# Kernel tuning notes

Hardware: AMD Instinct MI355X
Metric: run time of the kernel (lower is better)

## Reference

```python
import jax, jax.numpy as jnp
import numpy as np

B, L, D, H = 2, 4096, 768, 12
Dh = D // H


def setup_inputs() -> dict:
    key = jax.random.key(0)
    k1, k2, k3 = jax.random.split(key, 3)
    x = jax.random.normal(k1, (B, L, D), dtype=jnp.float32)
    Wqkv = jax.random.normal(k2, (D, 3 * D), dtype=jnp.float32) * 0.02
    bqkv = jnp.zeros((3 * D,), dtype=jnp.float32)
    Wo = jax.random.normal(k3, (D, D), dtype=jnp.float32) * 0.02
    bo = jnp.zeros((D,), dtype=jnp.float32)
    return {"x": x, "Wqkv": Wqkv, "bqkv": bqkv, "Wo": Wo, "bo": bo}


def reference(x, Wqkv, bqkv, Wo, bo):
    Bs, Ls, Ds = x.shape
    # fused QKV projection
    qkv = x @ Wqkv + bqkv  # [B, L, 3D]
    q, k, v = jnp.split(qkv, 3, axis=2)
    q = q.reshape(Bs, Ls, H, Dh)
    k = k.reshape(Bs, Ls, H, Dh)
    v = v.reshape(Bs, Ls, H, Dh)
    # scaled dot-product attention with causal mask (fp32 softmax, as flax dpa with dtype=float32)
    scale = 1.0 / np.sqrt(Dh)
    scores = jnp.einsum('bqhd,bkhd->bhqk', q, k) * scale  # [B, H, L, L]
    causal = jnp.tril(jnp.ones((Ls, Ls), dtype=bool))
    big_neg = jnp.finfo(jnp.float32).min
    scores = jnp.where(causal[None, None, :, :], scores, big_neg)
    attn = jax.nn.softmax(scores, axis=-1)
    y = jnp.einsum('bhqk,bkhd->bqhd', attn, v)  # [B, L, H, Dh]
    y = y.reshape(Bs, Ls, Ds)
    # output projection
    return y @ Wo + bo
```

## Files before the change

### kernel.cpp

```cpp
#include <hip/hip_runtime.h>
#include <hip/hip_bf16.h>
#include <stdint.h>

#define BB 2
#define LL 4096
#define DD 768
#define HH 12
#define DH 64
#define MM (BB * LL)
#define NQKV (3 * DD)
#define KK 768
#define PLANE ((size_t)BB * HH * LL * DH)
#define SQSCALE 0.1803368801111204f

typedef __attribute__((ext_vector_type(8))) short bf16x8;
typedef __attribute__((ext_vector_type(4))) float f32x4;

__device__ __forceinline__ float bf2f(uint16_t u) {
  union { uint32_t u; float f; } c; c.u = ((uint32_t)u) << 16; return c.f;
}
__device__ __forceinline__ uint16_t f2bf(float f) {
  union { float f; uint32_t u; } c; c.f = f;
  return (uint16_t)((c.u + 0x7FFFu + ((c.u >> 16) & 1u)) >> 16);
}
__device__ __forceinline__ uint32_t cvt2(float a, float b) {
  __hip_bfloat162 h = __float22bfloat162_rn(make_float2(a, b));
  union { __hip_bfloat162 h; uint32_t u; } c; c.h = h; return c.u;
}
#if __has_builtin(__builtin_amdgcn_exp2f)
__device__ __forceinline__ float fexp2(float x) { return __builtin_amdgcn_exp2f(x); }
#else
__device__ __forceinline__ float fexp2(float x) {
  float r;
  asm volatile("v_exp_f32 %0, %1\ns_nop 0" : "=v"(r) : "v"(x));
  return r;
}
#endif

union H8 { uint16_t h[8]; uint32_t w[4]; uint4 v; };
union B8 { uint2 d[2]; bf16x8 v; };

template <bool F32>
__device__ __forceinline__ H8 load8(const void* p, size_t idx) {
  H8 r;
  if (F32) {
    const float* f = (const float*)p + idx;
    float4 a = *(const float4*)f;
    float4 b = *(const float4*)(f + 4);
    r.w[0] = cvt2(a.x, a.y); r.w[1] = cvt2(a.z, a.w);
    r.w[2] = cvt2(b.x, b.y); r.w[3] = cvt2(b.z, b.w);
  } else {
    r.v = *(const uint4*)((const uint16_t*)p + idx);
  }
  return r;
}

__device__ __forceinline__ void g2l16(const uint16_t* g, uint16_t* l) {
  __builtin_amdgcn_global_load_lds((const __attribute__((address_space(1))) void*)g,
                                   (__attribute__((address_space(3))) void*)l,
                                   16, 0, 0);
}

__global__ void detect_k(const uint16_t* __restrict__ x, int* __restrict__ flag) {
  __shared__ int cnt;
  if (threadIdx.x == 0) cnt = 0;
  __syncthreads();
  int c = 0;
  for (int i = threadIdx.x; i < 4096; i += 256) {
    int e = (x[i] >> 7) & 0xFF;
    if (e == 0xFF || e > 133 || e < 100) c++;
  }
  atomicAdd(&cnt, c);
  __syncthreads();
  if (threadIdx.x == 0) *flag = (cnt > 512) ? 1 : 0;
}

__global__ __launch_bounds__(256) void prep_k(const void* __restrict__ x,
                                              uint16_t* __restrict__ xbf,
                                              const void* __restrict__ Wqkv,
                                              uint16_t* __restrict__ wqkvT,
                                              const void* __restrict__ Wo,
                                              uint16_t* __restrict__ woT,
                                              const int* __restrict__ flag) {
  __shared__ uint16_t Ts[64][65];
  const int fl = *flag;
  const int id = blockIdx.x;
  const int tid = threadIdx.x;
  if (id < 768) {
    size_t base = (size_t)id * 1024 + tid;
#pragma unroll
    for (int j = 0; j < 4; ++j) {
      size_t i = base + j * 256;
      H8 v = fl ? load8<true>(x, i * 8) : load8<false>(x, i * 8);
      *(uint4*)(xbf + i * 8) = v.v;
    }
    return;
  }
  const void* W;
  uint16_t* WT;
  int N, widx;
  if (id < 1200) { W = Wqkv; WT = wqkvT; N = NQKV; widx = id - 768; }
  else           { W = Wo;   WT = woT;   N = DD;   widx = id - 1200; }
  const int nb = N / 64;
  const int n0 = (widx % nb) * 64, k0 = (widx / nb) * 64;
#pragma unroll
  for (int j = 0; j < 16; ++j) {
    int idx = tid + j * 256;
    int r = idx >> 6, c = idx & 63;
    size_t gi = (size_t)(k0 + r) * N + n0 + c;
    float v = fl ? ((const float*)W)[gi] : bf2f(((const uint16_t*)W)[gi]);
    Ts[c][r] = f2bf(v);
  }
  __syncthreads();
#pragma unroll
  for (int j = 0; j < 16; ++j) {
    int idx = tid + j * 256;
    int n = idx >> 6, k = idx & 63;
    WT[(size_t)(n0 + n) * KK + k0 + k] = Ts[n][k];
  }
}

__device__ __forceinline__ void gemm128_core(const uint16_t* __restrict__ A,
                                             const uint16_t* __restrict__ BT,
                                             int m0, int n0,
                                             uint16_t* As, uint16_t* Bs,
                                             f32x4 acc[4][4]) {
  const int tid = threadIdx.x, lane = tid & 63, w = tid >> 6;
  const int quad = lane >> 4, c16 = lane & 15;
  const int wm = w >> 1, wn = w & 1;
  const int srow = lane >> 2, schunk = lane & 3;
  const int rsw = (c16 >> 1) & 3;
  for (int k0 = 0; k0 < KK; k0 += 32) {
#pragma unroll
    for (int i = 0; i < 2; ++i) {
      int row = w * 32 + i * 16 + srow;
      int gch = schunk ^ ((row >> 1) & 3);
      g2l16(A + (size_t)(m0 + row) * KK + k0 + gch * 8, As + (w * 32 + i * 16) * 32);
      g2l16(BT + (size_t)(n0 + row) * KK + k0 + gch * 8, Bs + (w * 32 + i * 16) * 32);
    }
    __syncthreads();
    bf16x8 a[4], b[4];
#pragma unroll
    for (int i = 0; i < 4; ++i) {
      a[i] = *(const bf16x8*)(As + (wm * 64 + i * 16 + c16) * 32 + ((quad ^ rsw) * 8));
      b[i] = *(const bf16x8*)(Bs + (wn * 64 + i * 16 + c16) * 32 + ((quad ^ rsw) * 8));
    }
#pragma unroll
    for (int i = 0; i < 4; ++i)
#pragma unroll
      for (int f = 0; f < 4; ++f)
        acc[i][f] = __builtin_amdgcn_mfma_f32_16x16x32_bf16(a[i], b[f], acc[i][f], 0, 0, 0);
    __syncthreads();
  }
}

__global__ __launch_bounds__(256) void qkv128_k(const uint16_t* __restrict__ X,
                                                const uint16_t* __restrict__ WT,
                                                const void* __restrict__ bias,
                                                uint16_t* __restrict__ planes,
                                                const int* __restrict__ flag) {
  __shared__ __align__(16) uint16_t smem[8704];
  uint16_t* As = smem;
  uint16_t* Bs = smem + 4096;
  const int fl = *flag;
  const int m0 = blockIdx.x * 128, n0 = blockIdx.y * 128;
  f32x4 acc[4][4];
#pragma unroll
  for (int i = 0; i < 4; ++i)
#pragma unroll
    for (int f = 0; f < 4; ++f) acc[i][f] = (f32x4){0.f, 0.f, 0.f, 0.f};
  gemm128_core(X, WT, m0, n0, As, Bs, acc);

  const int tid = threadIdx.x, lane = tid & 63, w = tid >> 6;
  const int quad = lane >> 4, c16 = lane & 15;
  const int wm = w >> 1, wn = w & 1;
  const int which = (n0 >= 2 * DD) ? 2 : (n0 >= DD ? 1 : 0);

  if (which < 2) {
    uint16_t* dst = planes + (size_t)which * PLANE;
    const float sc = (which == 0) ? SQSCALE : 1.0f;
#pragma unroll
    for (int f = 0; f < 4; ++f) {
      int n = n0 + wn * 64 + f * 16 + c16;
      float bv = fl ? ((const float*)bias)[n] : bf2f(((const uint16_t*)bias)[n]);
      int rem = n - which * DD;
      int hh = rem >> 6, dd = rem & 63;
#pragma unroll
      for (int i = 0; i < 4; ++i) {
        uint32_t pa = cvt2((acc[i][f][0] + bv) * sc, (acc[i][f][1] + bv) * sc);
        uint32_t pb = cvt2((acc[i][f][2] + bv) * sc, (acc[i][f][3] + bv) * sc);
        int m = m0 + wm * 64 + i * 16 + quad * 4;
        int b = m >> 12, l = m & (LL - 1);
        uint16_t* base = dst + ((size_t)(b * HH + hh) * LL + l) * DH + dd;
        base[0 * DH] = (uint16_t)pa;
        base[1 * DH] = (uint16_t)(pa >> 16);
        base[2 * DH] = (uint16_t)pb;
        base[3 * DH] = (uint16_t)(pb >> 16);
      }
    }
  } else {
    uint16_t (*Ts)[136] = reinterpret_cast<uint16_t(*)[136]>(smem);
    uint16_t* vtp = planes + 2 * PLANE;
    const int l0 = m0 & (LL - 1), bb = m0 >> 12;
    for (int half = 0; half < 2; ++half) {
      __syncthreads();
      if (wn == half) {
#pragma unroll
        for (int f = 0; f < 4; ++f) {
          int n = n0 + half * 64 + f * 16 + c16;
          float bv = fl ? ((const float*)bias)[n] : bf2f(((const uint16_t*)bias)[n]);
#pragma unroll
          for (int i = 0; i < 4; ++i) {
            uint32_t pa = cvt2(acc[i][f][0] + bv, acc[i][f][1] + bv);
            uint32_t pb = cvt2(acc[i][f][2] + bv, acc[i][f][3] + bv);
            *(uint2*)(&Ts[f * 16 + c16][wm * 64 + i * 16 + quad * 4]) = make_uint2(pa, pb);
          }
        }
      }
      __syncthreads();
#pragma unroll
      for (int j = 0; j < 4; ++j) {
        int idx = tid + j * 256;
        int nl = idx >> 4, ch = idx & 15;
        int rem = n0 + half * 64 + nl - 2 * DD;
        int hh = rem >> 6, dd = rem & 63;
        uint4 val = *(const uint4*)(&Ts[nl][ch * 8]);
        *(uint4*)(vtp + ((size_t)(bb * HH + hh) * DH + dd) * LL + l0 + ch * 8) = val;
      }
    }
  }
}

__global__ __launch_bounds__(256, 3) void attn_k(const uint16_t* __restrict__ planes,
                                                 uint16_t* __restrict__ y) {
  __shared__ __align__(16) uint16_t Ks[2][128 * 64];
  __shared__ __align__(16) uint16_t Vt[64 * 128];
  const int id = blockIdx.x;
  const int p = id / 24;
  const int bh = id % 24;
  const uint16_t* qb = planes + (size_t)bh * LL * DH;
  const uint16_t* kb = qb + PLANE;
  const uint16_t* vtb = planes + 2 * PLANE + (size_t)bh * DH * LL;
  const int tid = threadIdx.x, lane = tid & 63, wv = tid >> 6;
  const int quad = lane >> 4, c16 = lane & 15;
  const int swf = c16 & 7;
  const int b = bh / HH, hh = bh - b * HH;

  int koff[4];
  {
    int cp = lane & 7;
#pragma unroll
    for (int i = 0; i < 4; ++i) {
      int row = wv * 32 + i * 8 + (lane >> 3);
      koff[i] = row * 64 + ((cp ^ (row & 7)) * 8);
    }
  }
  const int kdst = wv * 32 * 64;

  const int kg = ((tid >> 2) & 1) | ((tid & 1) << 1);
  const int dr = ((tid >> 1) & 1) | (((tid >> 4) & 1) << 1) |
                 (((tid >> 3) & 1) << 2) | ((tid >> 5) << 3);
  const int swd = dr & 7;
  int vwoff[4][2];
#pragma unroll
  for (int j = 0; j < 4; ++j) {
#pragma unroll
    for (int h = 0; h < 2; ++h) {
      int ks = (kg + 4 * j) * 8 + 4 * h;
      int G = ks >> 6, ks6 = ks & 63;
      int ch = ((ks6 & 32) >> 3) + ((ks6 >> 2) & 3);
      int f4 = ((ks6 >> 4) & 1) * 4;
      vwoff[j][h] = dr * 128 + G * 64 + ((ch ^ swd ^ (G << 2)) * 8) + f4;
    }
  }

  B8 ones;
  ones.d[0] = make_uint2(0x3F803F80u, 0x3F803F80u);
  ones.d[1] = make_uint2(0x3F803F80u, 0x3F803F80u);

  for (int pass = 0; pass < 2; ++pass) {
    const int qi = pass ? p : 63 - p;
    const int nt = (qi + 2) >> 1;
    const int q0 = qi * 64;
    const size_t qoff = (size_t)(q0 + wv * 16 + c16) * DH;
    bf16x8 qf0 = *(const bf16x8*)(qb + qoff + quad * 8);
    bf16x8 qf1 = *(const bf16x8*)(qb + qoff + 32 + quad * 8);

    f32x4 o[4], lacc = (f32x4){0.f, 0.f, 0.f, 0.f};
#pragma unroll
    for (int g = 0; g < 4; ++g) o[g] = (f32x4){0.f, 0.f, 0.f, 0.f};

    const uint16_t* ksrc = kb;
    const uint16_t* vp = vtb + (size_t)dr * LL + kg * 8;
    uint4 vrg[4];
#pragma unroll
    for (int i = 0; i < 4; ++i) g2l16(ksrc + koff[i], Ks[0] + kdst + i * 512);
#pragma unroll
    for (int j = 0; j < 4; ++j) vrg[j] = *(const uint4*)(vp + j * 32);
    ksrc += 128 * DH; vp += 128;

    for (int t = 0; t < nt; ++t) {
      const uint16_t* kd = Ks[t & 1];
      uint16_t* knx = Ks[(t + 1) & 1];
      __syncthreads();
#pragma unroll
      for (int j = 0; j < 4; ++j) {
        *(uint2*)(Vt + vwoff[j][0]) = make_uint2(vrg[j].x, vrg[j].y);
        *(uint2*)(Vt + vwoff[j][1]) = make_uint2(vrg[j].z, vrg[j].w);
      }
      __syncthreads();
      if (t + 1 < nt) {
#pragma unroll
        for (int i = 0; i < 4; ++i) g2l16(ksrc + koff[i], knx + kdst + i * 512);
#pragma unroll
        for (int j = 0; j < 4; ++j) vrg[j] = *(const uint4*)(vp + j * 32);
        ksrc += 128 * DH; vp += 128;
      }

      const int qg = q0 + wv * 16 + c16;
      B8 pk[4];
#pragma unroll
      for (int h2 = 0; h2 < 2; ++h2) {
        f32x4 s[4];
        __builtin_amdgcn_s_setprio(1);
#pragma unroll
        for (int f = 0; f < 4; ++f) {
          const uint16_t* krow = kd + (h2 * 64 + f * 16 + c16) * 64;
          bf16x8 k0f = *(const bf16x8*)(krow + ((quad ^ swf) * 8));
          bf16x8 k1f = *(const bf16x8*)(krow + (((quad + 4) ^ swf) * 8));
          f32x4 z = {0.f, 0.f, 0.f, 0.f};
          z = __builtin_amdgcn_mfma_f32_16x16x32_bf16(k0f, qf0, z, 0, 0, 0);
          z = __builtin_amdgcn_mfma_f32_16x16x32_bf16(k1f, qf1, z, 0, 0, 0);
          s[f] = z;
        }
        __builtin_amdgcn_s_setprio(0);
        if (t == nt - 1) {
#pragma unroll
          for (int f = 0; f < 4; ++f) {
            int key0 = t * 128 + h2 * 64 + f * 16 + quad * 4;
#pragma unroll
            for (int r = 0; r < 4; ++r) {
              float pv = fexp2(s[f][r]);
              s[f][r] = (key0 + r <= qg) ? pv : 0.f;
            }
          }
        } else {
#pragma unroll
          for (int f = 0; f < 4; ++f)
#pragma unroll
            for (int r = 0; r < 4; ++r) s[f][r] = fexp2(s[f][r]);
        }
        pk[2 * h2].d[0] = make_uint2(cvt2(s[0][0], s[0][1]), cvt2(s[0][2], s[0][3]));
        pk[2 * h2].d[1] = make_uint2(cvt2(s[1][0], s[1][1]), cvt2(s[1][2], s[1][3]));
        pk[2 * h2 + 1].d[0] = make_uint2(cvt2(s[2][0], s[2][1]), cvt2(s[2][2], s[2][3]));
        pk[2 * h2 + 1].d[1] = make_uint2(cvt2(s[3][0], s[3][1]), cvt2(s[3][2], s[3][3]));
      }
      __builtin_amdgcn_s_setprio(1);
#pragma unroll
      for (int h = 0; h < 4; ++h)
        lacc = __builtin_amdgcn_mfma_f32_16x16x32_bf16(pk[h].v, ones.v, lacc, 0, 0, 0);
#pragma unroll
      for (int g = 0; g < 4; ++g) {
        const uint16_t* vrow = Vt + (g * 16 + c16) * 128;
#pragma unroll
        for (int sl = 0; sl < 4; ++sl) {
          int G = sl >> 1;
          int chunk = (quad + 4 * (sl & 1)) ^ swf ^ (G << 2);
          bf16x8 vv = *(const bf16x8*)(vrow + G * 64 + chunk * 8);
          o[g] = __builtin_amdgcn_mfma_f32_16x16x32_bf16(pk[sl].v, vv, o[g], 0, 0, 0);
        }
      }
      __builtin_amdgcn_s_setprio(0);
    }

    float inv[4];
#pragma unroll
    for (int r = 0; r < 4; ++r) inv[r] = 1.f / lacc[r];
#pragma unroll
    for (int g = 0; g < 4; ++g) {
      uint32_t pa = cvt2(o[g][0] * inv[0], o[g][1] * inv[1]);
      uint32_t pb = cvt2(o[g][2] * inv[2], o[g][3] * inv[3]);
      int l = q0 + wv * 16 + quad * 4;
      uint16_t* base = y + ((size_t)(b * LL + l)) * DD + hh * DH + g * 16 + c16;
      base[0 * DD] = (uint16_t)pa;
      base[1 * DD] = (uint16_t)(pa >> 16);
      base[2 * DD] = (uint16_t)pb;
      base[3 * DD] = (uint16_t)(pb >> 16);
    }
    __syncthreads();
  }
}

__global__ __launch_bounds__(256) void out64_k(const uint16_t* __restrict__ Y,
                                               const uint16_t* __restrict__ WT,
                                               const void* __restrict__ bias,
                                               void* __restrict__ out,
                                               const int* __restrict__ flag) {
  __shared__ __align__(16) uint16_t As[128 * 32];
  __shared__ __align__(16) uint16_t Bs[64 * 32];
  const int fl = *flag;
  const int m0 = blockIdx.x * 128, n0 = blockIdx.y * 64;
  const int tid = threadIdx.x, lane = tid & 63, w = tid >> 6;
  const int quad = lane >> 4, c16 = lane & 15;
  const int srow = lane >> 2, schunk = lane & 3;
  const int rsw = (c16 >> 1) & 3;
  f32x4 acc[2][4];
#pragma unroll
  for (int i = 0; i < 2; ++i)
#pragma unroll
    for (int f = 0; f < 4; ++f) acc[i][f] = (f32x4){0.f, 0.f, 0.f, 0.f};
  for (int k0 = 0; k0 < KK; k0 += 32) {
#pragma unroll
    for (int i = 0; i < 2; ++i) {
      int row = w * 32 + i * 16 + srow;
      int gch = schunk ^ ((row >> 1) & 3);
      g2l16(Y + (size_t)(m0 + row) * KK + k0 + gch * 8, As + (w * 32 + i * 16) * 32);
    }
    {
      int row = w * 16 + srow;
      int gch = schunk ^ ((row >> 1) & 3);
      g2l16(WT + (size_t)(n0 + row) * KK + k0 + gch * 8, Bs + (w * 16) * 32);
    }
    __syncthreads();
    bf16x8 a[2], bfr[4];
#pragma unroll
    for (int i = 0; i < 2; ++i)
      a[i] = *(const bf16x8*)(As + (w * 32 + i * 16 + c16) * 32 + ((quad ^ rsw) * 8));
#pragma unroll
    for (int f = 0; f < 4; ++f)
      bfr[f] = *(const bf16x8*)(Bs + (f * 16 + c16) * 32 + ((quad ^ rsw) * 8));
#pragma unroll
    for (int i = 0; i < 2; ++i)
#pragma unroll
      for (int f = 0; f < 4; ++f)
        acc[i][f] = __builtin_amdgcn_mfma_f32_16x16x32_bf16(a[i], bfr[f], acc[i][f], 0, 0, 0);
    __syncthreads();
  }
#pragma unroll
  for (int f = 0; f < 4; ++f) {
    int n = n0 + f * 16 + c16;
    float bv = fl ? ((const float*)bias)[n] : bf2f(((const uint16_t*)bias)[n]);
#pragma unroll
    for (int i = 0; i < 2; ++i) {
      int m = m0 + w * 32 + i * 16 + quad * 4;
      if (fl) {
        float* base = (float*)out + (size_t)m * DD + n;
#pragma unroll
        for (int r = 0; r < 4; ++r) base[r * DD] = acc[i][f][r] + bv;
      } else {
        uint32_t pa = cvt2(acc[i][f][0] + bv, acc[i][f][1] + bv);
        uint32_t pb = cvt2(acc[i][f][2] + bv, acc[i][f][3] + bv);
        uint16_t* base = (uint16_t*)out + (size_t)m * DD + n;
        base[0 * DD] = (uint16_t)pa;
        base[1 * DD] = (uint16_t)(pa >> 16);
        base[2 * DD] = (uint16_t)pb;
        base[3 * DD] = (uint16_t)(pb >> 16);
      }
    }
  }
}

extern "C" void kernel_launch(void* const* d_in, const int* in_sizes, int n_in,
                              void* d_out, int out_size, void* d_ws, size_t ws_size,
                              hipStream_t stream) {
  const void* x    = d_in[0];
  const void* Wqkv = d_in[1];
  const void* bqkv = d_in[2];
  const void* Wo   = d_in[3];
  const void* bo   = d_in[4];
  int* flagp = (int*)d_ws;
  uint16_t* planes = (uint16_t*)((char*)d_ws + 64);
  uint16_t* y_ws   = planes + 3 * PLANE;
  uint16_t* wqkvT  = y_ws + (size_t)MM * DD;
  uint16_t* woT    = wqkvT + (size_t)NQKV * KK;
  uint16_t* xbf    = y_ws;

  detect_k<<<1, 256, 0, stream>>>((const uint16_t*)x, flagp);
  prep_k<<<1344, 256, 0, stream>>>(x, xbf, Wqkv, wqkvT, Wo, woT, flagp);
  qkv128_k<<<dim3(MM / 128, NQKV / 128), 256, 0, stream>>>(xbf, wqkvT, bqkv, planes, flagp);
  attn_k<<<dim3(768), 256, 0, stream>>>(planes, y_ws);
  out64_k<<<dim3(MM / 128, DD / 64), 256, 0, stream>>>(y_ws, woT, bo, d_out, flagp);
}
```

Before: 246.8 us.

## Split attention waves over key halves and query pairs with LDS reduction

Changes the work split inside the attention block. Each wave now handles two 16-row query subtiles against one 64-key half of the 128-key tile, instead of one query subtile against all 128 keys. K fragments loaded from LDS are reused across two query subtiles and each V fragment feeds two MFMAs, which cuts LDS read traffic per MFMA. The cost is a cross-wave reduction through shared memory (reusing the K buffer) at the end of each pass, two extra barriers, and higher register pressure under the 3-block occupancy bound.

```diff
diff --git a/kernel.cpp b/kernel.cpp
--- a/kernel.cpp
+++ b/kernel.cpp
@@ -244,6 +244,8 @@
   const int tid = threadIdx.x, lane = tid & 63, wv = tid >> 6;
   const int quad = lane >> 4, c16 = lane & 15;
   const int swf = c16 & 7;
+  const int qsub = wv & 1;
+  const int kg = wv >> 1;
   const int b = bh / HH, hh = bh - b * HH;
 
   int koff[4];
@@ -257,41 +259,51 @@
   }
   const int kdst = wv * 32 * 64;
 
-  const int kg = ((tid >> 2) & 1) | ((tid & 1) << 1);
-  const int dr = ((tid >> 1) & 1) | (((tid >> 4) & 1) << 1) |
-                 (((tid >> 3) & 1) << 2) | ((tid >> 5) << 3);
-  const int swd = dr & 7;
+  const int vkg = ((tid >> 2) & 1) | ((tid & 1) << 1);
+  const int vdr = ((tid >> 1) & 1) | (((tid >> 4) & 1) << 1) |
+                  (((tid >> 3) & 1) << 2) | ((tid >> 5) << 3);
+  const int swd = vdr & 7;
   int vwoff[4][2];
 #pragma unroll
   for (int j = 0; j < 4; ++j) {
 #pragma unroll
     for (int h = 0; h < 2; ++h) {
-      int ks = (kg + 4 * j) * 8 + 4 * h;
+      int ks = (vkg + 4 * j) * 8 + 4 * h;
       int G = ks >> 6, ks6 = ks & 63;
       int ch = ((ks6 & 32) >> 3) + ((ks6 >> 2) & 3);
       int f4 = ((ks6 >> 4) & 1) * 4;
-      vwoff[j][h] = dr * 128 + G * 64 + ((ch ^ swd ^ (G << 2)) * 8) + f4;
+      vwoff[j][h] = vdr * 128 + G * 64 + ((ch ^ swd ^ (G << 2)) * 8) + f4;
     }
   }
 
   B8 ones;
   ones.d[0] = make_uint2(0x3F803F80u, 0x3F803F80u);
   ones.d[1] = make_uint2(0x3F803F80u, 0x3F803F80u);
+
+  float* osm = (float*)(&Ks[0][0]);
 
   for (int pass = 0; pass < 2; ++pass) {
     const int qi = pass ? p : 63 - p;
     const int nt = (qi + 2) >> 1;
     const int q0 = qi * 64;
-    const size_t qoff = (size_t)(q0 + wv * 16 + c16) * DH;
-    bf16x8 qf0 = *(const bf16x8*)(qb + qoff + quad * 8);
-    bf16x8 qf1 = *(const bf16x8*)(qb + qoff + 32 + quad * 8);
-
-    f32x4 o[4], lacc = (f32x4){0.f, 0.f, 0.f, 0.f};
-#pragma unroll
-    for (int g = 0; g < 4; ++g) o[g] = (f32x4){0.f, 0.f, 0.f, 0.f};
+    bf16x8 qf[2][2];
+#pragma unroll
+    for (int s = 0; s < 2; ++s) {
+      size_t qoff = (size_t)(q0 + qsub * 32 + s * 16 + c16) * DH;
+      qf[s][0] = *(const bf16x8*)(qb + qoff + quad * 8);
+      qf[s][1] = *(const bf16x8*)(qb + qoff + 32 + quad * 8);
+    }
+
+    f32x4 o[2][4], la[2];
+#pragma unroll
+    for (int s = 0; s < 2; ++s) {
+      la[s] = (f32x4){0.f, 0.f, 0.f, 0.f};
+#pragma unroll
+      for (int g = 0; g < 4; ++g) o[s][g] = (f32x4){0.f, 0.f, 0.f, 0.f};
+    }
 
     const uint16_t* ksrc = kb;
-    const uint16_t* vp = vtb + (size_t)dr * LL + kg * 8;
+    const uint16_t* vp = vtb + (size_t)vdr * LL + vkg * 8;
     uint4 vrg[4];
 #pragma unroll
     for (int i = 0; i < 4; ++i) g2l16(ksrc + koff[i], Ks[0] + kdst + i * 512);
@@ -317,75 +329,103 @@
         ksrc += 128 * DH; vp += 128;
       }
 
-      const int qg = q0 + wv * 16 + c16;
-      B8 pk[4];
-#pragma unroll
-      for (int h2 = 0; h2 < 2; ++h2) {
-        f32x4 s[4];
+      bf16x8 kfr[4][2];
+#pragma unroll
+      for (int f = 0; f < 4; ++f) {
+        const uint16_t* krow = kd + (kg * 64 + f * 16 + c16) * 64;
+        kfr[f][0] = *(const bf16x8*)(krow + ((quad ^ swf) * 8));
+        kfr[f][1] = *(const bf16x8*)(krow + (((quad + 4) ^ swf) * 8));
+      }
+      B8 pk[2][2];
+#pragma unroll
+      for (int s = 0; s < 2; ++s) {
+        f32x4 sv[4];
         __builtin_amdgcn_s_setprio(1);
 #pragma unroll
         for (int f = 0; f < 4; ++f) {
-          const uint16_t* krow = kd + (h2 * 64 + f * 16 + c16) * 64;
-          bf16x8 k0f = *(const bf16x8*)(krow + ((quad ^ swf) * 8));
-          bf16x8 k1f = *(const bf16x8*)(krow + (((quad + 4) ^ swf) * 8));
           f32x4 z = {0.f, 0.f, 0.f, 0.f};
-          z = __builtin_amdgcn_mfma_f32_16x16x32_bf16(k0f, qf0, z, 0, 0, 0);
-          z = __builtin_amdgcn_mfma_f32_16x16x32_bf16(k1f, qf1, z, 0, 0, 0);
-          s[f] = z;
+          z = __builtin_amdgcn_mfma_f32_16x16x32_bf16(kfr[f][0], qf[s][0], z, 0, 0, 0);
+          z = __builtin_amdgcn_mfma_f32_16x16x32_bf16(kfr[f][1], qf[s][1], z, 0, 0, 0);
+          sv[f] = z;
         }
         __builtin_amdgcn_s_setprio(0);
+        const int qg = q0 + qsub * 32 + s * 16 + c16;
         if (t == nt - 1) {
 #pragma unroll
           for (int f = 0; f < 4; ++f) {
-            int key0 = t * 128 + h2 * 64 + f * 16 + quad * 4;
+            int key0 = t * 128 + kg * 64 + f * 16 + quad * 4;
 #pragma unroll
             for (int r = 0; r < 4; ++r) {
-              float pv = fexp2(s[f][r]);
-              s[f][r] = (key0 + r <= qg) ? pv : 0.f;
+              float pv = fexp2(sv[f][r]);
+              sv[f][r] = (key0 + r <= qg) ? pv : 0.f;
             }
           }
         } else {
 #pragma unroll
           for (int f = 0; f < 4; ++f)
 #pragma unroll
-            for (int r = 0; r < 4; ++r) s[f][r] = fexp2(s[f][r]);
+            for (int r = 0; r < 4; ++r) sv[f][r] = fexp2(sv[f][r]);
         }
-        pk[2 * h2].d[0] = make_uint2(cvt2(s[0][0], s[0][1]), cvt2(s[0][2], s[0][3]));
-        pk[2 * h2].d[1] = make_uint2(cvt2(s[1][0], s[1][1]), cvt2(s[1][2], s[1][3]));
-        pk[2 * h2 + 1].d[0] = make_uint2(cvt2(s[2][0], s[2][1]), cvt2(s[2][2], s[2][3]));
-        pk[2 * h2 + 1].d[1] = make_uint2(cvt2(s[3][0], s[3][1]), cvt2(s[3][2], s[3][3]));
+        pk[s][0].d[0] = make_uint2(cvt2(sv[0][0], sv[0][1]), cvt2(sv[0][2], sv[0][3]));
+        pk[s][0].d[1] = make_uint2(cvt2(sv[1][0], sv[1][1]), cvt2(sv[1][2], sv[1][3]));
+        pk[s][1].d[0] = make_uint2(cvt2(sv[2][0], sv[2][1]), cvt2(sv[2][2], sv[2][3]));
+        pk[s][1].d[1] = make_uint2(cvt2(sv[3][0], sv[3][1]), cvt2(sv[3][2], sv[3][3]));
       }
       __builtin_amdgcn_s_setprio(1);
 #pragma unroll
-      for (int h = 0; h < 4; ++h)
-        lacc = __builtin_amdgcn_mfma_f32_16x16x32_bf16(pk[h].v, ones.v, lacc, 0, 0, 0);
+      for (int s = 0; s < 2; ++s)
+#pragma unroll
+        for (int j = 0; j < 2; ++j)
+          la[s] = __builtin_amdgcn_mfma_f32_16x16x32_bf16(pk[s][j].v, ones.v, la[s], 0, 0, 0);
 #pragma unroll
       for (int g = 0; g < 4; ++g) {
-        const uint16_t* vrow = Vt + (g * 16 + c16) * 128;
-#pragma unroll
-        for (int sl = 0; sl < 4; ++sl) {
-          int G = sl >> 1;
-          int chunk = (quad + 4 * (sl & 1)) ^ swf ^ (G << 2);
-          bf16x8 vv = *(const bf16x8*)(vrow + G * 64 + chunk * 8);
-          o[g] = __builtin_amdgcn_mfma_f32_16x16x32_bf16(pk[sl].v, vv, o[g], 0, 0, 0);
+        const uint16_t* vrow = Vt + (g * 16 + c16) * 128 + kg * 64;
+#pragma unroll
+        for (int j = 0; j < 2; ++j) {
+          int chunk = (quad + 4 * j) ^ swf ^ (kg << 2);
+          bf16x8 vv = *(const bf16x8*)(vrow + chunk * 8);
+          o[0][g] = __builtin_amdgcn_mfma_f32_16x16x32_bf16(pk[0][j].v, vv, o[0][g], 0, 0, 0);
+          o[1][g] = __builtin_amdgcn_mfma_f32_16x16x32_bf16(pk[1][j].v, vv, o[1][g], 0, 0, 0);
         }
       }
       __builtin_amdgcn_s_setprio(0);
     }
 
-    float inv[4];
-#pragma unroll
-    for (int r = 0; r < 4; ++r) inv[r] = 1.f / lacc[r];
-#pragma unroll
-    for (int g = 0; g < 4; ++g) {
-      uint32_t pa = cvt2(o[g][0] * inv[0], o[g][1] * inv[1]);
-      uint32_t pb = cvt2(o[g][2] * inv[2], o[g][3] * inv[3]);
-      int l = q0 + wv * 16 + quad * 4;
-      uint16_t* base = y + ((size_t)(b * LL + l)) * DD + hh * DH + g * 16 + c16;
-      base[0 * DD] = (uint16_t)pa;
-      base[1 * DD] = (uint16_t)(pa >> 16);
-      base[2 * DD] = (uint16_t)pb;
-      base[3 * DD] = (uint16_t)(pb >> 16);
+    __syncthreads();
+    if (kg == 1) {
+#pragma unroll
+      for (int s = 0; s < 2; ++s) {
+#pragma unroll
+        for (int g = 0; g < 4; ++g)
+          *(f32x4*)(osm + ((qsub * 8 + s * 4 + g) * 64 + lane) * 4) = o[s][g];
+        *(f32x4*)(osm + 4096 + ((qsub * 2 + s) * 64 + lane) * 4) = la[s];
+      }
+    }
+    __syncthreads();
+    if (kg == 0) {
+#pragma unroll
+      for (int s = 0; s < 2; ++s) {
+        f32x4 lp = *(const f32x4*)(osm + 4096 + ((qsub * 2 + s) * 64 + lane) * 4);
+        float inv[4];
+#pragma unroll
+        for (int r = 0; r < 4; ++r) inv[r] = 1.f / (la[s][r] + lp[r]);
+        int l = q0 + qsub * 32 + s * 16 + quad * 4;
+#pragma unroll
+        for (int g = 0; g < 4; ++g) {
+          f32x4 op = *(const f32x4*)(osm + ((qsub * 8 + s * 4 + g) * 64 + lane) * 4);
+          float v0 = (o[s][g][0] + op[0]) * inv[0];
+          float v1 = (o[s][g][1] + op[1]) * inv[1];
+          float v2 = (o[s][g][2] + op[2]) * inv[2];
+          float v3 = (o[s][g][3] + op[3]) * inv[3];
+          uint32_t pa = cvt2(v0, v1);
+          uint32_t pb = cvt2(v2, v3);
+          uint16_t* base = y + ((size_t)(b * LL + l)) * DD + hh * DH + g * 16 + c16;
+          base[0 * DD] = (uint16_t)pa;
+          base[1 * DD] = (uint16_t)(pa >> 16);
+          base[2 * DD] = (uint16_t)pb;
+          base[3 * DD] = (uint16_t)(pb >> 16);
+        }
+      }
     }
     __syncthreads();
   }
```

After: 238.7 us. -3.3%, faster.
